# Performance work log

Hardware: AMD Instinct MI355X
Metric: run time of the kernel (lower is better)

The kernel has to match this reference:

```python
import jax, jax.numpy as jnp
import numpy as np

N_NODES = 100000
NEG_SLOPE = 0.2  # PyG GATConv default


def gat_conv(x, W, b, a_src, a_dst, src, dst, n):
    # Linear transform: [N, out]
    h = x @ W
    # Per-node attention logits (heads=1): scalar per node
    s_src = h @ a_src  # contribution from message source x_j
    s_dst = h @ a_dst  # contribution from message target x_i
    # Per-edge raw attention, LeakyReLU as in PyG
    alpha = jax.nn.leaky_relu(s_src[src] + s_dst[dst], negative_slope=NEG_SLOPE)
    # Segment softmax over incoming edges of each destination node
    amax = jax.ops.segment_max(alpha, dst, num_segments=n)
    ex = jnp.exp(alpha - amax[dst])
    denom = jax.ops.segment_sum(ex, dst, num_segments=n)
    coef = ex / denom[dst]  # [E+N] attention coefficients
    # Scatter-aggregate weighted source features to destinations
    out = jax.ops.segment_sum(h[src] * coef[:, None], dst, num_segments=n)
    return out + b


def setup_inputs() -> dict:
    key = jax.random.key(0)
    k_x, k_e, k_w = jax.random.split(key, 3)
    n, e, d_in, d_h, n_layers = N_NODES, 1600000, 128, 128, 3
    x = jax.random.normal(k_x, (n, d_in), dtype=jnp.float32)
    edge_index = jax.random.randint(k_e, (2, e), 0, n, dtype=jnp.int64)
    ks = jax.random.split(k_w, 4)
    glorot = float(np.sqrt(6.0 / (d_in + d_h)))
    Ws = jax.random.uniform(ks[0], (n_layers, d_in, d_h), jnp.float32, -glorot, glorot)
    a_g = float(np.sqrt(6.0 / (d_h + 1)))
    a_srcs = jax.random.uniform(ks[1], (n_layers, d_h), jnp.float32, -a_g, a_g)
    a_dsts = jax.random.uniform(ks[2], (n_layers, d_h), jnp.float32, -a_g, a_g)
    bs = jnp.zeros((n_layers, d_h), dtype=jnp.float32)
    return {"x": x, "edge_index": edge_index, "Ws": Ws, "bs": bs,
            "a_srcs": a_srcs, "a_dsts": a_dsts}


def reference(x, edge_index, Ws, bs, a_srcs, a_dsts):
    n = x.shape[0]
    # add self loops (PyG GATConv default add_self_loops=True)
    loop = jnp.arange(n, dtype=edge_index.dtype)
    src = jnp.concatenate([edge_index[0], loop])
    dst = jnp.concatenate([edge_index[1], loop])
    h = x
    for i in range(Ws.shape[0]):
        h = jax.nn.relu(gat_conv(h, Ws[i], bs[i], a_srcs[i], a_dsts[i], src, dst, n))
    return h
```

## Files before the change

### kernel.cpp

```cpp
#include <hip/hip_runtime.h>
#include <hip/hip_bf16.h>
#include <cstdint>
#include <cstddef>

#define D 128
#define NEG_SLOPE 0.2f

__device__ __forceinline__ float leaky(float x) { return x > 0.f ? x : NEG_SLOPE * x; }


__global__ void gat_count_deg(const int* __restrict__ ei, int* __restrict__ cursor, int E) {
    int e = blockIdx.x * 256 + threadIdx.x;
    if (e < E) atomicAdd(&cursor[ei[E + e]], 1);
}

__global__ void gat_chunk_sum(const int* __restrict__ deg, int* __restrict__ partial, int n) {
    __shared__ int sm[256];
    int t = threadIdx.x, base = blockIdx.x * 512;
    int s = 0;
    if (base + t < n)       s += deg[base + t];
    if (base + 256 + t < n) s += deg[base + 256 + t];
    sm[t] = s; __syncthreads();
    for (int off = 128; off; off >>= 1) { if (t < off) sm[t] += sm[t + off]; __syncthreads(); }
    if (t == 0) partial[blockIdx.x] = sm[0];
}

__global__ void gat_scan_partials(const int* __restrict__ partial, int* __restrict__ chunkoff,
                                  int* __restrict__ rowptr, int nchunks, int n) {
    __shared__ int sm[256];
    int t = threadIdx.x;
    int v = (t < nchunks) ? partial[t] : 0;
    sm[t] = v; __syncthreads();
    for (int off = 1; off < 256; off <<= 1) {
        int x = (t >= off) ? sm[t - off] : 0;
        __syncthreads();
        sm[t] += x;
        __syncthreads();
    }
    chunkoff[t] = sm[t] - v;
    if (t == 255) rowptr[n] = sm[255];
}

__global__ void gat_chunk_scan(int* __restrict__ cursor, int* __restrict__ rowptr,
                               const int* __restrict__ chunkoff, int n) {
    __shared__ int sm[256];
    int t = threadIdx.x, base = blockIdx.x * 512;
    int i0 = base + 2 * t, i1 = i0 + 1;
    int d0 = (i0 < n) ? cursor[i0] : 0;
    int d1 = (i1 < n) ? cursor[i1] : 0;
    int s = d0 + d1;
    sm[t] = s; __syncthreads();
    for (int off = 1; off < 256; off <<= 1) {
        int x = (t >= off) ? sm[t - off] : 0;
        __syncthreads();
        sm[t] += x;
        __syncthreads();
    }
    int excl = sm[t] - s + chunkoff[blockIdx.x];
    if (i0 < n) { rowptr[i0] = excl;      cursor[i0] = excl; }
    if (i1 < n) { rowptr[i1] = excl + d0; cursor[i1] = excl + d0; }
}

__global__ void gat_scatter(const int* __restrict__ ei, int* __restrict__ cursor,
                            int* __restrict__ csr, int E) {
    int e = blockIdx.x * 256 + threadIdx.x;
    if (e < E) {
        int s = ei[e], d = ei[E + e];
        int p = atomicAdd(&cursor[d], 1);
        csr[p] = s;
    }
}

__launch_bounds__(256)
__global__ void gat_gemm_s(const float* __restrict__ A, const float* __restrict__ W,
                           const float* __restrict__ aS, const float* __restrict__ aD,
                           float* __restrict__ H, float* __restrict__ sS, float* __restrict__ sD,
                           int n) {
    __shared__ float At[32][68];
    __shared__ float Wt[32][136];
    int t = threadIdx.x;
    int tn = t & 15, tm = t >> 4;
    int r0 = blockIdx.x * 64;

    float c[4][8];
#pragma unroll
    for (int r = 0; r < 4; ++r)
#pragma unroll
        for (int j = 0; j < 8; ++j) c[r][j] = 0.f;

    for (int k0 = 0; k0 < D; k0 += 32) {
        int row = t >> 3;
        int c4 = (t & 7) * 4;
#pragma unroll
        for (int h = 0; h < 2; ++h) {
            int rr = row + h * 32;
            int gr = r0 + rr;
            float4 v;
            if (gr < n) v = *(const float4*)&A[(size_t)gr * D + k0 + c4];
            else { v.x = v.y = v.z = v.w = 0.f; }
            At[c4 + 0][rr] = v.x; At[c4 + 1][rr] = v.y;
            At[c4 + 2][rr] = v.z; At[c4 + 3][rr] = v.w;
        }
#pragma unroll
        for (int i = 0; i < 4; ++i) {
            int idx = t + i * 256;
            int k = idx >> 5;
            int cw = (idx & 31) * 4;
            *(float4*)&Wt[k][cw] = *(const float4*)&W[(size_t)(k0 + k) * D + cw];
        }
        __syncthreads();
#pragma unroll
        for (int kk = 0; kk < 32; ++kk) {
            float4 a4 = *(const float4*)&At[kk][tm * 4];
            float4 b0 = *(const float4*)&Wt[kk][tn * 8];
            float4 b1 = *(const float4*)&Wt[kk][tn * 8 + 4];
            float a_[4] = {a4.x, a4.y, a4.z, a4.w};
            float b_[8] = {b0.x, b0.y, b0.z, b0.w, b1.x, b1.y, b1.z, b1.w};
#pragma unroll
            for (int r = 0; r < 4; ++r)
#pragma unroll
                for (int j = 0; j < 8; ++j) c[r][j] += a_[r] * b_[j];
        }
        __syncthreads();
    }

    float as_[8], ad_[8];
#pragma unroll
    for (int j = 0; j < 8; ++j) { as_[j] = aS[tn * 8 + j]; ad_[j] = aD[tn * 8 + j]; }
    float pS[4], pD[4];
#pragma unroll
    for (int r = 0; r < 4; ++r) {
        int gr = r0 + tm * 4 + r;
        pS[r] = 0.f; pD[r] = 0.f;
#pragma unroll
        for (int j = 0; j < 8; ++j) { pS[r] += as_[j] * c[r][j]; pD[r] += ad_[j] * c[r][j]; }
        if (gr < n) {
            float4 v0; v0.x = c[r][0]; v0.y = c[r][1]; v0.z = c[r][2]; v0.w = c[r][3];
            float4 v1; v1.x = c[r][4]; v1.y = c[r][5]; v1.z = c[r][6]; v1.w = c[r][7];
            *(float4*)&H[(size_t)gr * D + tn * 8]     = v0;
            *(float4*)&H[(size_t)gr * D + tn * 8 + 4] = v1;
        }
    }
#pragma unroll
    for (int off = 1; off < 16; off <<= 1) {
#pragma unroll
        for (int r = 0; r < 4; ++r) {
            pS[r] += __shfl_xor(pS[r], off);
            pD[r] += __shfl_xor(pD[r], off);
        }
    }
    if (tn == 0) {
#pragma unroll
        for (int r = 0; r < 4; ++r) {
            int gr = r0 + tm * 4 + r;
            if (gr < n) { sS[gr] = pS[r]; sD[gr] = pD[r]; }
        }
    }
}

__launch_bounds__(256)
__global__ void gat_agg(const float* __restrict__ H, const int* __restrict__ rowptr,
                        const int* __restrict__ csr, const float* __restrict__ sS,
                        const float* __restrict__ sD, const float* __restrict__ b,
                        float* __restrict__ O, int n) {
    int v = blockIdx.x * 4 + (threadIdx.x >> 6);
    if (v >= n) return;
    int lane = threadIdx.x & 63;
    int st = rowptr[v], en = rowptr[v + 1];
    float sdv = sD[v];
    float aself = leaky(sS[v] + sdv);

    int i0 = st + lane;
    int u0 = (i0 < en) ? csr[i0] : 0;
    float s0 = (i0 < en) ? leaky(sS[u0] + sdv) : -3e38f;

    float m = fmaxf(aself, s0);
    for (int i = i0 + 64; i < en; i += 64) {
        int u = csr[i];
        m = fmaxf(m, leaky(sS[u] + sdv));
    }
#pragma unroll
    for (int off = 32; off; off >>= 1) m = fmaxf(m, __shfl_xor(m, off));

    float w0 = (i0 < en) ? __expf(s0 - m) : 0.f;
    float wself = __expf(aself - m);
    float t = w0;
#pragma unroll
    for (int off = 32; off; off >>= 1) t += __shfl_xor(t, off);
    float l = wself + t;

    int ch = lane * 2;
    float2 hv = *(const float2*)&H[(size_t)v * D + ch];
    float ax0 = wself * hv.x, ay0 = wself * hv.y;
    float ax1 = 0.f, ay1 = 0.f, ax2 = 0.f, ay2 = 0.f, ax3 = 0.f, ay3 = 0.f;

    int cn = en - st; if (cn > 64) cn = 64;
    int j = 0;
    for (; j + 4 <= cn; j += 4) {
        int uu0 = __shfl(u0, j),     uu1 = __shfl(u0, j + 1);
        int uu2 = __shfl(u0, j + 2), uu3 = __shfl(u0, j + 3);
        float ww0 = __shfl(w0, j),     ww1 = __shfl(w0, j + 1);
        float ww2 = __shfl(w0, j + 2), ww3 = __shfl(w0, j + 3);
        float2 h0 = *(const float2*)&H[(size_t)uu0 * D + ch];
        float2 h1 = *(const float2*)&H[(size_t)uu1 * D + ch];
        float2 h2 = *(const float2*)&H[(size_t)uu2 * D + ch];
        float2 h3 = *(const float2*)&H[(size_t)uu3 * D + ch];
        ax0 += ww0 * h0.x; ay0 += ww0 * h0.y;
        ax1 += ww1 * h1.x; ay1 += ww1 * h1.y;
        ax2 += ww2 * h2.x; ay2 += ww2 * h2.y;
        ax3 += ww3 * h3.x; ay3 += ww3 * h3.y;
    }
    for (; j < cn; ++j) {
        int uu = __shfl(u0, j);
        float ww = __shfl(w0, j);
        float2 hu = *(const float2*)&H[(size_t)uu * D + ch];
        ax0 += ww * hu.x; ay0 += ww * hu.y;
    }

    for (int c = st + 64; c < en; c += 64) {
        int i = c + lane;
        int u = (i < en) ? csr[i] : 0;
        float s = (i < en) ? leaky(sS[u] + sdv) : 0.f;
        float w = (i < en) ? __expf(s - m) : 0.f;
        float tt = w;
#pragma unroll
        for (int off = 32; off; off >>= 1) tt += __shfl_xor(tt, off);
        l += tt;
        int cc = en - c; if (cc > 64) cc = 64;
        int k = 0;
        for (; k + 4 <= cc; k += 4) {
            int uu0 = __shfl(u, k),     uu1 = __shfl(u, k + 1);
            int uu2 = __shfl(u, k + 2), uu3 = __shfl(u, k + 3);
            float ww0 = __shfl(w, k),     ww1 = __shfl(w, k + 1);
            float ww2 = __shfl(w, k + 2), ww3 = __shfl(w, k + 3);
            float2 h0 = *(const float2*)&H[(size_t)uu0 * D + ch];
            float2 h1 = *(const float2*)&H[(size_t)uu1 * D + ch];
            float2 h2 = *(const float2*)&H[(size_t)uu2 * D + ch];
            float2 h3 = *(const float2*)&H[(size_t)uu3 * D + ch];
            ax0 += ww0 * h0.x; ay0 += ww0 * h0.y;
            ax1 += ww1 * h1.x; ay1 += ww1 * h1.y;
            ax2 += ww2 * h2.x; ay2 += ww2 * h2.y;
            ax3 += ww3 * h3.x; ay3 += ww3 * h3.y;
        }
        for (; k < cc; ++k) {
            int uu = __shfl(u, k);
            float ww = __shfl(w, k);
            float2 hu = *(const float2*)&H[(size_t)uu * D + ch];
            ax0 += ww * hu.x; ay0 += ww * hu.y;
        }
    }

    float accx = (ax0 + ax1) + (ax2 + ax3);
    float accy = (ay0 + ay1) + (ay2 + ay3);
    float inv = 1.0f / l;
    float2 bb = *(const float2*)&b[ch];
    float2 o;
    o.x = fmaxf(accx * inv + bb.x, 0.f);
    o.y = fmaxf(accy * inv + bb.y, 0.f);
    *(float2*)&O[(size_t)v * D + ch] = o;
}


extern "C" void kernel_launch(void* const* d_in, const int* in_sizes, int n_in,
                              void* d_out, int out_size, void* d_ws, size_t ws_size,
                              hipStream_t stream) {
    const float* x  = (const float*)d_in[0];
    const int*   ei = (const int*)d_in[1];
    const float* Ws = (const float*)d_in[2];
    const float* bs = (const float*)d_in[3];
    const float* aS = (const float*)d_in[4];
    const float* aD = (const float*)d_in[5];
    float* out = (float*)d_out;

    int N = in_sizes[0] / D;
    int E = in_sizes[1] / 2;
    int L = in_sizes[2] / (D * D);

    char* w = (char*)d_ws;
    auto alloc = [&](size_t bytes) { char* p = w; w += (bytes + 255) & ~(size_t)255; return p; };
    int*   cursor   = (int*)alloc((size_t)N * 4);
    int*   rowptr   = (int*)alloc((size_t)(N + 1) * 4);
    int*   partial  = (int*)alloc(256 * 4);
    int*   chunkoff = (int*)alloc(256 * 4);
    int*   csr      = (int*)alloc((size_t)E * 4);
    float* sS       = (float*)alloc((size_t)N * 4);
    float* sD       = (float*)alloc((size_t)N * 4);
    float* H        = (float*)alloc((size_t)N * D * 4);

    hipMemsetAsync(cursor, 0, (size_t)N * 4, stream);
    int nch = (N + 511) / 512;
    gat_count_deg<<<(E + 255) / 256, 256, 0, stream>>>(ei, cursor, E);
    gat_chunk_sum<<<nch, 256, 0, stream>>>(cursor, partial, N);
    gat_scan_partials<<<1, 256, 0, stream>>>(partial, chunkoff, rowptr, nch, N);
    gat_chunk_scan<<<nch, 256, 0, stream>>>(cursor, rowptr, chunkoff, N);
    gat_scatter<<<(E + 255) / 256, 256, 0, stream>>>(ei, cursor, csr, E);

    const float* in = x;
    for (int l = 0; l < L; ++l) {
        gat_gemm_s<<<(N + 63) / 64, 256, 0, stream>>>(
            in, Ws + (size_t)l * D * D, aS + (size_t)l * D, aD + (size_t)l * D,
            H, sS, sD, N);
        gat_agg<<<(N + 3) / 4, 256, 0, stream>>>(H, rowptr, csr, sS, sD,
                                                 bs + (size_t)l * D, out, N);
        in = out;
    }
}
```

Before: 810.5 us.

## Build CSR via two-pass bucket sort with shared-memory atomics

Replaces the per-node global-atomic degree count, multi-kernel scan and global-atomic scatter with a two-level bucket sort. Edges are first binned by destination block of 1024 nodes using shared-memory histograms and a padded global cursor per bucket, staged in the H buffer as packed (src, local dst) words. Each bucket is then sorted locally in shared memory to produce rowptr and csr. The aim is to cut random global atomics and kernel launches, at the cost of an extra pass over the edges, a packing scheme that assumes N under 131072 and at most 128 buckets, and a single-threaded serial bucket scan.

Result: faster. 710.9 us (-12.3%).

```diff
diff --git a/kernel.cpp b/kernel.cpp
--- a/kernel.cpp
+++ b/kernel.cpp
@@ -5,69 +5,109 @@
 
 #define D 128
 #define NEG_SLOPE 0.2f
+#define NBMAX 128
+#define BSH 10
+#define CPAD 16
 
 __device__ __forceinline__ float leaky(float x) { return x > 0.f ? x : NEG_SLOPE * x; }
 
 
-__global__ void gat_count_deg(const int* __restrict__ ei, int* __restrict__ cursor, int E) {
-    int e = blockIdx.x * 256 + threadIdx.x;
-    if (e < E) atomicAdd(&cursor[ei[E + e]], 1);
-}
-
-__global__ void gat_chunk_sum(const int* __restrict__ deg, int* __restrict__ partial, int n) {
-    __shared__ int sm[256];
-    int t = threadIdx.x, base = blockIdx.x * 512;
-    int s = 0;
-    if (base + t < n)       s += deg[base + t];
-    if (base + 256 + t < n) s += deg[base + 256 + t];
-    sm[t] = s; __syncthreads();
-    for (int off = 128; off; off >>= 1) { if (t < off) sm[t] += sm[t + off]; __syncthreads(); }
-    if (t == 0) partial[blockIdx.x] = sm[0];
-}
-
-__global__ void gat_scan_partials(const int* __restrict__ partial, int* __restrict__ chunkoff,
-                                  int* __restrict__ rowptr, int nchunks, int n) {
-    __shared__ int sm[256];
+__global__ void gat_hist(const int* __restrict__ ei, int* __restrict__ gcount,
+                         int E, int NB) {
+    __shared__ int h[NBMAX];
     int t = threadIdx.x;
-    int v = (t < nchunks) ? partial[t] : 0;
-    sm[t] = v; __syncthreads();
+    if (t < NBMAX) h[t] = 0;
+    __syncthreads();
+    for (int e = blockIdx.x * 256 + t; e < E; e += gridDim.x * 256)
+        atomicAdd(&h[ei[E + e] >> BSH], 1);
+    __syncthreads();
+    if (t < NB && h[t]) atomicAdd(&gcount[t * CPAD], h[t]);
+}
+
+__global__ void gat_bases(const int* __restrict__ gcount, int* __restrict__ bases,
+                          int* __restrict__ cursor, int* __restrict__ rowptr,
+                          int NB, int N, int E) {
+    if (threadIdx.x == 0) {
+        int s = 0;
+        for (int b = 0; b < NB; ++b) {
+            bases[b] = s;
+            cursor[b * CPAD] = s;
+            s += gcount[b * CPAD];
+        }
+        rowptr[N] = E;
+    }
+}
+
+__launch_bounds__(256)
+__global__ void gat_bucket(const int* __restrict__ ei, int* __restrict__ cursor,
+                           int* __restrict__ stg, int E) {
+    __shared__ int hist[NBMAX], lcur[NBMAX], rbase[NBMAX];
+    int t = threadIdx.x;
+    int e0 = blockIdx.x * 2048;
+    if (t < NBMAX) hist[t] = 0;
+    __syncthreads();
+    int pk[8], bk[8];
+#pragma unroll
+    for (int j = 0; j < 8; ++j) {
+        int e = e0 + t + j * 256;
+        if (e < E) {
+            int s = ei[e], d = ei[E + e];
+            bk[j] = d >> BSH;
+            pk[j] = s | ((d & ((1 << BSH) - 1)) << 17);
+            atomicAdd(&hist[bk[j]], 1);
+        } else bk[j] = -1;
+    }
+    __syncthreads();
+    if (t < NBMAX) {
+        lcur[t] = 0;
+        if (hist[t]) rbase[t] = atomicAdd(&cursor[t * CPAD], hist[t]);
+    }
+    __syncthreads();
+#pragma unroll
+    for (int j = 0; j < 8; ++j) {
+        if (bk[j] >= 0) {
+            int p = rbase[bk[j]] + atomicAdd(&lcur[bk[j]], 1);
+            stg[p] = pk[j];
+        }
+    }
+}
+
+__launch_bounds__(256)
+__global__ void gat_build(const int* __restrict__ stg, const int* __restrict__ gcount,
+                          const int* __restrict__ bases, int* __restrict__ rowptr,
+                          int* __restrict__ csr, int N) {
+    __shared__ int deg[1 << BSH];
+    __shared__ int cur[1 << BSH];
+    __shared__ int part[256];
+    int b = blockIdx.x, t = threadIdx.x;
+    int base = bases[b], cnt = gcount[b * CPAD];
+#pragma unroll
+    for (int j = 0; j < (1 << BSH) / 256; ++j) deg[t + j * 256] = 0;
+    __syncthreads();
+    for (int i = t; i < cnt; i += 256) atomicAdd(&deg[stg[base + i] >> 17], 1);
+    __syncthreads();
+    int d0 = deg[t * 4], d1 = deg[t * 4 + 1], d2 = deg[t * 4 + 2], d3 = deg[t * 4 + 3];
+    int tsum = d0 + d1 + d2 + d3;
+    part[t] = tsum; __syncthreads();
     for (int off = 1; off < 256; off <<= 1) {
-        int x = (t >= off) ? sm[t - off] : 0;
+        int x = (t >= off) ? part[t - off] : 0;
         __syncthreads();
-        sm[t] += x;
+        part[t] += x;
         __syncthreads();
     }
-    chunkoff[t] = sm[t] - v;
-    if (t == 255) rowptr[n] = sm[255];
-}
-
-__global__ void gat_chunk_scan(int* __restrict__ cursor, int* __restrict__ rowptr,
-                               const int* __restrict__ chunkoff, int n) {
-    __shared__ int sm[256];
-    int t = threadIdx.x, base = blockIdx.x * 512;
-    int i0 = base + 2 * t, i1 = i0 + 1;
-    int d0 = (i0 < n) ? cursor[i0] : 0;
-    int d1 = (i1 < n) ? cursor[i1] : 0;
-    int s = d0 + d1;
-    sm[t] = s; __syncthreads();
-    for (int off = 1; off < 256; off <<= 1) {
-        int x = (t >= off) ? sm[t - off] : 0;
-        __syncthreads();
-        sm[t] += x;
-        __syncthreads();
-    }
-    int excl = sm[t] - s + chunkoff[blockIdx.x];
-    if (i0 < n) { rowptr[i0] = excl;      cursor[i0] = excl; }
-    if (i1 < n) { rowptr[i1] = excl + d0; cursor[i1] = excl + d0; }
-}
-
-__global__ void gat_scatter(const int* __restrict__ ei, int* __restrict__ cursor,
-                            int* __restrict__ csr, int E) {
-    int e = blockIdx.x * 256 + threadIdx.x;
-    if (e < E) {
-        int s = ei[e], d = ei[E + e];
-        int p = atomicAdd(&cursor[d], 1);
-        csr[p] = s;
+    int ex = part[t] - tsum;
+    int e0 = ex, e1 = ex + d0, e2 = e1 + d1, e3 = e2 + d2;
+    cur[t * 4] = e0; cur[t * 4 + 1] = e1; cur[t * 4 + 2] = e2; cur[t * 4 + 3] = e3;
+    int nb0 = b << BSH;
+    if (nb0 + t * 4     < N) rowptr[nb0 + t * 4]     = base + e0;
+    if (nb0 + t * 4 + 1 < N) rowptr[nb0 + t * 4 + 1] = base + e1;
+    if (nb0 + t * 4 + 2 < N) rowptr[nb0 + t * 4 + 2] = base + e2;
+    if (nb0 + t * 4 + 3 < N) rowptr[nb0 + t * 4 + 3] = base + e3;
+    __syncthreads();
+    for (int i = t; i < cnt; i += 256) {
+        int e = stg[base + i];
+        int p = atomicAdd(&cur[e >> 17], 1);
+        csr[base + p] = e & 0x1FFFF;
     }
 }
 
@@ -275,25 +315,25 @@
     int N = in_sizes[0] / D;
     int E = in_sizes[1] / 2;
     int L = in_sizes[2] / (D * D);
+    int NB = (N + (1 << BSH) - 1) >> BSH;
 
     char* w = (char*)d_ws;
     auto alloc = [&](size_t bytes) { char* p = w; w += (bytes + 255) & ~(size_t)255; return p; };
-    int*   cursor   = (int*)alloc((size_t)N * 4);
-    int*   rowptr   = (int*)alloc((size_t)(N + 1) * 4);
-    int*   partial  = (int*)alloc(256 * 4);
-    int*   chunkoff = (int*)alloc(256 * 4);
-    int*   csr      = (int*)alloc((size_t)E * 4);
-    float* sS       = (float*)alloc((size_t)N * 4);
-    float* sD       = (float*)alloc((size_t)N * 4);
-    float* H        = (float*)alloc((size_t)N * D * 4);
-
-    hipMemsetAsync(cursor, 0, (size_t)N * 4, stream);
-    int nch = (N + 511) / 512;
-    gat_count_deg<<<(E + 255) / 256, 256, 0, stream>>>(ei, cursor, E);
-    gat_chunk_sum<<<nch, 256, 0, stream>>>(cursor, partial, N);
-    gat_scan_partials<<<1, 256, 0, stream>>>(partial, chunkoff, rowptr, nch, N);
-    gat_chunk_scan<<<nch, 256, 0, stream>>>(cursor, rowptr, chunkoff, N);
-    gat_scatter<<<(E + 255) / 256, 256, 0, stream>>>(ei, cursor, csr, E);
+    int*   gcount = (int*)alloc((size_t)NBMAX * CPAD * 4);
+    int*   cursor = (int*)alloc((size_t)NBMAX * CPAD * 4);
+    int*   bases  = (int*)alloc((size_t)NBMAX * 4);
+    int*   rowptr = (int*)alloc((size_t)(N + 1) * 4);
+    int*   csr    = (int*)alloc((size_t)E * 4);
+    float* sS     = (float*)alloc((size_t)N * 4);
+    float* sD     = (float*)alloc((size_t)N * 4);
+    float* H      = (float*)alloc((size_t)N * D * 4);
+    int*   stg    = (int*)H;
+
+    hipMemsetAsync(gcount, 0, (size_t)NBMAX * CPAD * 4, stream);
+    gat_hist  <<<512, 256, 0, stream>>>(ei, gcount, E, NB);
+    gat_bases <<<1, 64, 0, stream>>>(gcount, bases, cursor, rowptr, NB, N, E);
+    gat_bucket<<<(E + 2047) / 2048, 256, 0, stream>>>(ei, cursor, stg, E);
+    gat_build <<<NB, 256, 0, stream>>>(stg, gcount, bases, rowptr, csr, N);
 
     const float* in = x;
     for (int l = 0; l < L; ++l) {
```
